# Kernel optimization log

Hardware: AMD Instinct MI355X
Metric: run time of the kernel (lower is better)

Reference implementation:

```python
import math
import jax, jax.numpy as jnp
import numpy as np

ALPHA = 0.2                         # LeakyReLU slope
LAMBDA_INIT = 0.8 - 0.6 * math.exp(-0.3 * 1)  # lambda_init_fn(depth=1)
NEG_INF = -9e15
EPS_LN = 1e-5

B, N, IN_F, OUT_F = 4, 2048, 512, 512
INTERNAL = OUT_F // 2
REL_DIM = 10
NUM_REL = 6


def setup_inputs() -> dict:
    key = jax.random.key(0)
    ks = jax.random.split(key, 16)
    xav = lambda k, shape, fan: jax.random.normal(k, shape, jnp.float32) * (1.414 * math.sqrt(2.0 / fan))
    h = jax.random.normal(ks[0], (B, N, IN_F), jnp.float32)
    adj = jax.random.randint(ks[1], (B, N, N), 0, NUM_REL, jnp.int32)
    W = xav(ks[2], (IN_F, OUT_F), IN_F + OUT_F)
    a_left_pos = xav(ks[3], (INTERNAL,), INTERNAL + 1)
    a_right_pos = xav(ks[4], (INTERNAL,), INTERNAL + 1)
    a_left_neg = xav(ks[5], (INTERNAL,), INTERNAL + 1)
    a_right_neg = xav(ks[6], (INTERNAL,), INTERNAL + 1)
    rel_table = jax.random.normal(ks[7], (NUM_REL, REL_DIM), jnp.float32)
    a_rel_pos = xav(ks[8], (REL_DIM,), REL_DIM + 1)
    a_rel_neg = xav(ks[9], (REL_DIM,), REL_DIM + 1)
    ll1 = 0.1 * jax.random.normal(ks[10], (INTERNAL,), jnp.float32)
    lr1 = 0.1 * jax.random.normal(ks[11], (INTERNAL,), jnp.float32)
    ll2 = 0.1 * jax.random.normal(ks[12], (INTERNAL,), jnp.float32)
    lr2 = 0.1 * jax.random.normal(ks[13], (INTERNAL,), jnp.float32)
    ln_gamma = jnp.ones((OUT_F,), jnp.float32)
    ln_beta = jnp.zeros((OUT_F,), jnp.float32)
    return dict(h=h, adj=adj, W=W, a_left_pos=a_left_pos, a_right_pos=a_right_pos,
                a_left_neg=a_left_neg, a_right_neg=a_right_neg, rel_table=rel_table,
                a_rel_pos=a_rel_pos, a_rel_neg=a_rel_neg, ll1=ll1, lr1=lr1,
                ll2=ll2, lr2=lr2, ln_gamma=ln_gamma, ln_beta=ln_beta)


def _leaky(x):
    return jnp.where(x >= 0, x, ALPHA * x)


def reference(h, adj, W, a_left_pos, a_right_pos, a_left_neg, a_right_neg,
              rel_table, a_rel_pos, a_rel_neg, ll1, lr1, ll2, lr2,
              ln_gamma, ln_beta):
    # Projection: Wh [B,N,out] -> split into pos/neg halves [B,N,internal]
    Wh = jnp.einsum('bni,io->bno', h, W)
    Bn, Nn, _ = Wh.shape
    Wh2 = Wh.reshape(Bn, Nn, 2, INTERNAL)
    Wh_pos, Wh_neg = Wh2[:, :, 0, :], Wh2[:, :, 1, :]

    # Additive GAT-style scores: e[b,i,j] = a_left.Wh[i] + a_right.Wh[j]
    e_pos = (Wh_pos @ a_left_pos)[:, :, None] + (Wh_pos @ a_right_pos)[:, None, :]
    e_neg = (Wh_neg @ a_left_neg)[:, :, None] + (Wh_neg @ a_right_neg)[:, None, :]

    # Relation-embedding bias: gather [B,N,N,rel_dim] then project to scalar
    rel_emb = rel_table[adj]                       # [B,N,N,R]
    e_pos = e_pos + rel_emb @ a_rel_pos
    e_neg = e_neg + rel_emb @ a_rel_neg

    mask = adj > 0
    att_pos = jax.nn.softmax(jnp.where(mask, _leaky(e_pos), NEG_INF), axis=2)
    att_neg = jax.nn.softmax(jnp.where(mask, _leaky(e_neg), NEG_INF), axis=2)

    lam = jnp.exp(jnp.sum(ll1 * lr1)) - jnp.exp(jnp.sum(ll2 * lr2)) + LAMBDA_INIT
    attention = att_pos - lam * att_neg            # dropout is identity (eval)

    Wh_v = jnp.concatenate([Wh_pos, Wh_neg], axis=-1)   # [B,N,out]
    h_prime = jnp.einsum('bij,bjd->bid', attention, Wh_v)

    mu = jnp.mean(h_prime, axis=-1, keepdims=True)
    var = jnp.mean(jnp.square(h_prime - mu), axis=-1, keepdims=True)
    h_prime = (h_prime - mu) / jnp.sqrt(var + EPS_LN) * ln_gamma + ln_beta
    h_prime = h_prime * (1 - LAMBDA_INIT)
    return jax.nn.gelu(h_prime, approximate=False), attention
```

## Files before the change

kernel.cpp:

```cpp
#include <hip/hip_runtime.h>
#include <hip/hip_bf16.h>


#define B_ 4
#define N_ 2048
#define F_ 512
#define ALPHA_ 0.2f
#define NEG_INF_ -9000000000000000.0f
#define EPS_LN_ 1e-5f

typedef __attribute__((ext_vector_type(8))) short bf16x8;
typedef __attribute__((ext_vector_type(4))) float f32x4;

#define HBF_OFF   0
#define WHT_OFF   0
#define WT_OFF    8388608
#define WH_OFF    8912896
#define HP_OFF    8912896
#define ATTBF_OFF 25690112
#define EL_OFF    59244544
#define SC_OFF    59375616
#define FLAG_OFF  59375680
#define CANON_OFF 59375744

#define C_ALP 0
#define C_ARP 256
#define C_ALN 512
#define C_ARN 768
#define C_REL 1024
#define C_ARELP 1084
#define C_ARELN 1094
#define C_LL1 1104
#define C_LR1 1360
#define C_LL2 1616
#define C_LR2 1872
#define C_GAM 2128
#define C_BET 2640

__device__ __forceinline__ float bf_as_f32(unsigned short u) {
    return __uint_as_float(((unsigned)u) << 16);
}
__device__ __forceinline__ float ldf(const void* p, long i, int isf32) {
    return isf32 ? ((const float*)p)[i] : bf_as_f32(((const unsigned short*)p)[i]);
}

__global__ void k_detect(const unsigned short* __restrict__ hraw, int* __restrict__ flag) {
    __shared__ float wmax[4];
    int tid = threadIdx.x, lane = tid & 63, wid = tid >> 6;
    float mx = 0.f;
    for (int i = tid; i < 8192; i += 256) {
        float v = fabsf(bf_as_f32(hraw[i]));
        if (v == v && v > mx) mx = v;
    }
    for (int off = 32; off; off >>= 1) mx = fmaxf(mx, __shfl_down(mx, off));
    if (lane == 0) wmax[wid] = mx;
    __syncthreads();
    if (tid == 0) {
        float m = fmaxf(fmaxf(wmax[0], wmax[1]), fmaxf(wmax[2], wmax[3]));
        flag[0] = (m > 1e10f) ? 1 : 0;
    }
}

__global__ __launch_bounds__(256) void k_conv_h(const void* __restrict__ h, const int* __restrict__ flag,
                                                __hip_bfloat16* __restrict__ hbf) {
    int fl = flag[0];
    int idx = blockIdx.x * 256 + threadIdx.x;
    hbf[idx] = __float2bfloat16(ldf(h, idx, fl));
}

__global__ __launch_bounds__(256) void k_conv_W(const void* __restrict__ W, const int* __restrict__ flag,
                                                __hip_bfloat16* __restrict__ Wt) {
    int fl = flag[0];
    int idx = blockIdx.x * 256 + threadIdx.x;
    int k = idx >> 9, o = idx & 511;
    Wt[o * 512 + k] = __float2bfloat16(ldf(W, idx, fl));
}

__global__ void k_conv_small(const void* alp, const void* arp, const void* aln, const void* arn,
                             const void* rel, const void* arelp, const void* areln,
                             const void* ll1, const void* lr1, const void* ll2, const void* lr2,
                             const void* gam, const void* bet,
                             const int* __restrict__ flag, float* __restrict__ canon) {
    int fl = flag[0];
    int tid = threadIdx.x;
    canon[C_ALP + tid] = ldf(alp, tid, fl);
    canon[C_ARP + tid] = ldf(arp, tid, fl);
    canon[C_ALN + tid] = ldf(aln, tid, fl);
    canon[C_ARN + tid] = ldf(arn, tid, fl);
    canon[C_LL1 + tid] = ldf(ll1, tid, fl);
    canon[C_LR1 + tid] = ldf(lr1, tid, fl);
    canon[C_LL2 + tid] = ldf(ll2, tid, fl);
    canon[C_LR2 + tid] = ldf(lr2, tid, fl);
    canon[C_GAM + tid] = ldf(gam, tid, fl);
    canon[C_GAM + 256 + tid] = ldf(gam, 256 + tid, fl);
    canon[C_BET + tid] = ldf(bet, tid, fl);
    canon[C_BET + 256 + tid] = ldf(bet, 256 + tid, fl);
    if (tid < 60) canon[C_REL + tid] = ldf(rel, tid, fl);
    if (tid < 10) { canon[C_ARELP + tid] = ldf(arelp, tid, fl); canon[C_ARELN + tid] = ldf(areln, tid, fl); }
}

__global__ void k_scalars(const float* __restrict__ canon, float* __restrict__ sc) {
    int lane = threadIdx.x;
    float s1 = 0.f, s2 = 0.f;
    for (int k = lane; k < 256; k += 64) {
        s1 += canon[C_LL1 + k] * canon[C_LR1 + k];
        s2 += canon[C_LL2 + k] * canon[C_LR2 + k];
    }
    for (int off = 32; off; off >>= 1) { s1 += __shfl_down(s1, off); s2 += __shfl_down(s2, off); }
    if (lane == 0) {
        float lam_init = 0.8f - 0.6f * expf(-0.3f);
        sc[0] = expf(s1) - expf(s2) + lam_init;
    }
    if (lane < 6) {
        float p = 0.f, n = 0.f;
        for (int d = 0; d < 10; ++d) {
            float rv = canon[C_REL + lane * 10 + d];
            p += rv * canon[C_ARELP + d];
            n += rv * canon[C_ARELN + d];
        }
        sc[1 + lane] = p;
        sc[7 + lane] = n;
    }
}

__global__ __launch_bounds__(256) void k_gemm_wh(const __hip_bfloat16* __restrict__ A,
                                                 const __hip_bfloat16* __restrict__ Bt,
                                                 float* __restrict__ C) {
    __shared__ short As[128][32];
    __shared__ short Bs[64][32];
    int tid = threadIdx.x, wid = tid >> 6, lane = tid & 63;
    int bm = blockIdx.x * 128, bn = blockIdx.y * 64;
    const short* Ag = (const short*)A;
    const short* Bg = (const short*)Bt;
    f32x4 acc[2][4] = {};
    for (int k0 = 0; k0 < 512; k0 += 32) {
        __syncthreads();
#pragma unroll
        for (int it = 0; it < 2; ++it) {
            int t = it * 256 + tid;
            int row = t >> 2, col8 = (t & 3) * 8;
            *(bf16x8*)&As[row][col8] = *(const bf16x8*)&Ag[(bm + row) * 512 + k0 + col8];
        }
        {
            int row = tid >> 2, col8 = (tid & 3) * 8;
            *(bf16x8*)&Bs[row][col8] = *(const bf16x8*)&Bg[(bn + row) * 512 + k0 + col8];
        }
        __syncthreads();
        int l15 = lane & 15, kh = (lane >> 4) * 8;
        bf16x8 af[2], bfr[4];
#pragma unroll
        for (int m = 0; m < 2; ++m) af[m] = *(const bf16x8*)&As[wid * 32 + m * 16 + l15][kh];
#pragma unroll
        for (int n = 0; n < 4; ++n) bfr[n] = *(const bf16x8*)&Bs[n * 16 + l15][kh];
#pragma unroll
        for (int m = 0; m < 2; ++m)
#pragma unroll
            for (int n = 0; n < 4; ++n)
                acc[m][n] = __builtin_amdgcn_mfma_f32_16x16x32_bf16(af[m], bfr[n], acc[m][n], 0, 0, 0);
    }
    int l15 = lane & 15, rg = (lane >> 4) * 4;
#pragma unroll
    for (int m = 0; m < 2; ++m)
#pragma unroll
        for (int n = 0; n < 4; ++n)
#pragma unroll
            for (int r = 0; r < 4; ++r) {
                int row = bm + wid * 32 + m * 16 + rg + r;
                int col = bn + n * 16 + l15;
                C[row * 512 + col] = acc[m][n][r];
            }
}

__global__ __launch_bounds__(256) void k_transWh(const float* __restrict__ Wh, __hip_bfloat16* __restrict__ Wht) {
    __shared__ float t[32][33];
    int b = blockIdx.z;
    int o0 = blockIdx.x * 32, j0 = blockIdx.y * 32;
    int tx = threadIdx.x & 31, ty = threadIdx.x >> 5;
#pragma unroll
    for (int r = 0; r < 4; ++r) {
        int j = j0 + ty + r * 8;
        t[ty + r * 8][tx] = Wh[(b * 2048 + j) * 512 + o0 + tx];
    }
    __syncthreads();
#pragma unroll
    for (int r = 0; r < 4; ++r) {
        int o = o0 + ty + r * 8;
        Wht[((long)b * 512 + o) * 2048 + j0 + tx] = __float2bfloat16(t[tx][ty + r * 8]);
    }
}

__global__ __launch_bounds__(256) void k_edots(const float* __restrict__ Wh, const float* __restrict__ canon,
                                               float* __restrict__ el) {
    int wid = threadIdx.x >> 6, lane = threadIdx.x & 63;
    int m = blockIdx.x * 4 + wid;
    float selp = 0.f, serp = 0.f, seln = 0.f, sern = 0.f;
#pragma unroll
    for (int t = 0; t < 4; ++t) {
        int k = t * 64 + lane;
        float wp = Wh[m * 512 + k];
        float wn = Wh[m * 512 + 256 + k];
        selp += wp * canon[C_ALP + k];
        serp += wp * canon[C_ARP + k];
        seln += wn * canon[C_ALN + k];
        sern += wn * canon[C_ARN + k];
    }
    for (int off = 32; off; off >>= 1) {
        selp += __shfl_down(selp, off); serp += __shfl_down(serp, off);
        seln += __shfl_down(seln, off); sern += __shfl_down(sern, off);
    }
    if (lane == 0) {
        el[m] = selp; el[8192 + m] = serp; el[16384 + m] = seln; el[24576 + m] = sern;
    }
}

__global__ __launch_bounds__(256) void k_attn(const int* __restrict__ adj,
                                              const float* __restrict__ el, const float* __restrict__ sc,
                                              float* __restrict__ att_f32,
                                              __hip_bfloat16* __restrict__ att_bf) {
    __shared__ float s_rp[6], s_rn[6], s_lam[1];
    __shared__ float rmp[4], rmn[4], rsp[4], rsn[4];
    int tid = threadIdx.x, lane = tid & 63, wid = tid >> 6;
    if (tid < 6) { s_rp[tid] = sc[1 + tid]; s_rn[tid] = sc[7 + tid]; }
    if (tid == 6) s_lam[0] = sc[0];
    int m = blockIdx.x, b = m >> 11;
    float elp = el[m], eln = el[16384 + m];
    const float* erp = el + 8192 + b * 2048;
    const float* ern = el + 24576 + b * 2048;
    const int* adjr = adj + (long)m * 2048;
    __syncthreads();
    float sp[8], sn[8];
    float mp = NEG_INF_, mn = NEG_INF_;
#pragma unroll
    for (int t = 0; t < 8; ++t) {
        int j = t * 256 + tid;
        int a = adjr[j];
        float ep = elp + erp[j] + s_rp[a];
        float en = eln + ern[j] + s_rn[a];
        ep = ep >= 0.f ? ep : ALPHA_ * ep;
        en = en >= 0.f ? en : ALPHA_ * en;
        sp[t] = a > 0 ? ep : NEG_INF_;
        sn[t] = a > 0 ? en : NEG_INF_;
        mp = fmaxf(mp, sp[t]); mn = fmaxf(mn, sn[t]);
    }
    for (int off = 32; off; off >>= 1) { mp = fmaxf(mp, __shfl_down(mp, off)); mn = fmaxf(mn, __shfl_down(mn, off)); }
    if (lane == 0) { rmp[wid] = mp; rmn[wid] = mn; }
    __syncthreads();
    mp = fmaxf(fmaxf(rmp[0], rmp[1]), fmaxf(rmp[2], rmp[3]));
    mn = fmaxf(fmaxf(rmn[0], rmn[1]), fmaxf(rmn[2], rmn[3]));
    float sump = 0.f, sumn = 0.f;
#pragma unroll
    for (int t = 0; t < 8; ++t) {
        sp[t] = expf(sp[t] - mp);
        sn[t] = expf(sn[t] - mn);
        sump += sp[t]; sumn += sn[t];
    }
    for (int off = 32; off; off >>= 1) { sump += __shfl_down(sump, off); sumn += __shfl_down(sumn, off); }
    if (lane == 0) { rsp[wid] = sump; rsn[wid] = sumn; }
    __syncthreads();
    sump = rsp[0] + rsp[1] + rsp[2] + rsp[3];
    sumn = rsn[0] + rsn[1] + rsn[2] + rsn[3];
    float ip = 1.0f / sump, inn = 1.0f / sumn;
    float lam = s_lam[0];
#pragma unroll
    for (int t = 0; t < 8; ++t) {
        float v = sp[t] * ip - lam * sn[t] * inn;
        long idx = (long)m * 2048 + t * 256 + tid;
        att_f32[idx] = v;
        att_bf[idx] = __float2bfloat16(v);
    }
}

__global__ __launch_bounds__(256) void k_hprime(const __hip_bfloat16* __restrict__ att,
                                                const __hip_bfloat16* __restrict__ Wht,
                                                float* __restrict__ HP) {
    __shared__ short As[128][32];
    __shared__ short Bs[64][32];
    int tid = threadIdx.x, wid = tid >> 6, lane = tid & 63;
    int b = blockIdx.z;
    int bm = blockIdx.x * 128, bn = blockIdx.y * 64;
    const short* Ag = (const short*)(att + (long)b * 2048 * 2048);
    const short* Bg = (const short*)(Wht + (long)b * 512 * 2048);
    f32x4 acc[2][4] = {};
    for (int k0 = 0; k0 < 2048; k0 += 32) {
        __syncthreads();
#pragma unroll
        for (int it = 0; it < 2; ++it) {
            int t = it * 256 + tid;
            int row = t >> 2, col8 = (t & 3) * 8;
            *(bf16x8*)&As[row][col8] = *(const bf16x8*)&Ag[(long)(bm + row) * 2048 + k0 + col8];
        }
        {
            int row = tid >> 2, col8 = (tid & 3) * 8;
            *(bf16x8*)&Bs[row][col8] = *(const bf16x8*)&Bg[(long)(bn + row) * 2048 + k0 + col8];
        }
        __syncthreads();
        int l15 = lane & 15, kh = (lane >> 4) * 8;
        bf16x8 af[2], bfr[4];
#pragma unroll
        for (int m = 0; m < 2; ++m) af[m] = *(const bf16x8*)&As[wid * 32 + m * 16 + l15][kh];
#pragma unroll
        for (int n = 0; n < 4; ++n) bfr[n] = *(const bf16x8*)&Bs[n * 16 + l15][kh];
#pragma unroll
        for (int m = 0; m < 2; ++m)
#pragma unroll
            for (int n = 0; n < 4; ++n)
                acc[m][n] = __builtin_amdgcn_mfma_f32_16x16x32_bf16(af[m], bfr[n], acc[m][n], 0, 0, 0);
    }
    int l15 = lane & 15, rg = (lane >> 4) * 4;
#pragma unroll
    for (int m = 0; m < 2; ++m)
#pragma unroll
        for (int n = 0; n < 4; ++n)
#pragma unroll
            for (int r = 0; r < 4; ++r) {
                int row = bm + wid * 32 + m * 16 + rg + r;
                int col = bn + n * 16 + l15;
                HP[((long)b * 2048 + row) * 512 + col] = acc[m][n][r];
            }
}

__global__ __launch_bounds__(256) void k_lngelu(const float* __restrict__ HP, const float* __restrict__ canon,
                                                float* __restrict__ out) {
    int wid = threadIdx.x >> 6, lane = threadIdx.x & 63;
    int m = blockIdx.x * 4 + wid;
    float x[8]; float s = 0.f, ss = 0.f;
#pragma unroll
    for (int t = 0; t < 8; ++t) {
        x[t] = HP[m * 512 + t * 64 + lane];
        s += x[t]; ss += x[t] * x[t];
    }
    for (int off = 32; off; off >>= 1) { s += __shfl_xor(s, off); ss += __shfl_xor(ss, off); }
    float mu = s * (1.0f / 512.0f);
    float var = ss * (1.0f / 512.0f) - mu * mu;
    float inv = rsqrtf(fmaxf(var, 0.0f) + EPS_LN_);
    float scale = 1.0f - (0.8f - 0.6f * expf(-0.3f));
#pragma unroll
    for (int t = 0; t < 8; ++t) {
        int k = t * 64 + lane;
        float y = (x[t] - mu) * inv * canon[C_GAM + k] + canon[C_BET + k];
        y *= scale;
        float g = 0.5f * y * (1.0f + erff(y * 0.70710678118654752f));
        out[m * 512 + k] = g;
    }
}

extern "C" void kernel_launch(void* const* d_in, const int* in_sizes, int n_in,
                              void* d_out, int out_size, void* d_ws, size_t ws_size,
                              hipStream_t stream) {
    const void* h   = d_in[0];
    const int*  adj = (const int*)d_in[1];
    const void* W   = d_in[2];
    const void* alp = d_in[3];
    const void* arp = d_in[4];
    const void* aln = d_in[5];
    const void* arn = d_in[6];
    const void* rel = d_in[7];
    const void* arelp = d_in[8];
    const void* areln = d_in[9];
    const void* ll1 = d_in[10];
    const void* lr1 = d_in[11];
    const void* ll2 = d_in[12];
    const void* lr2 = d_in[13];
    const void* gam = d_in[14];
    const void* bet = d_in[15];

    char* ws = (char*)d_ws;
    __hip_bfloat16* hbf   = (__hip_bfloat16*)(ws + HBF_OFF);
    __hip_bfloat16* Wt    = (__hip_bfloat16*)(ws + WT_OFF);
    float*          Wh    = (float*)(ws + WH_OFF);
    __hip_bfloat16* Wht   = (__hip_bfloat16*)(ws + WHT_OFF);
    __hip_bfloat16* attbf = (__hip_bfloat16*)(ws + ATTBF_OFF);
    float*          el    = (float*)(ws + EL_OFF);
    float*          sc    = (float*)(ws + SC_OFF);
    int*            flg   = (int*)(ws + FLAG_OFF);
    float*          can   = (float*)(ws + CANON_OFF);
    float*          HP    = (float*)(ws + HP_OFF);

    float* out_gelu = (float*)d_out;
    float* out_att  = out_gelu + (size_t)B_ * N_ * F_;

    k_detect<<<1, 256, 0, stream>>>((const unsigned short*)h, flg);
    k_conv_h<<<16384, 256, 0, stream>>>(h, flg, hbf);
    k_conv_W<<<1024, 256, 0, stream>>>(W, flg, Wt);
    k_conv_small<<<1, 256, 0, stream>>>(alp, arp, aln, arn, rel, arelp, areln,
                                        ll1, lr1, ll2, lr2, gam, bet, flg, can);
    k_scalars<<<1, 64, 0, stream>>>(can, sc);
    k_gemm_wh<<<dim3(64, 8), 256, 0, stream>>>(hbf, Wt, Wh);
    k_transWh<<<dim3(16, 64, 4), 256, 0, stream>>>(Wh, Wht);
    k_edots<<<2048, 256, 0, stream>>>(Wh, can, el);
    k_attn<<<8192, 256, 0, stream>>>(adj, el, sc, out_att, attbf);
    k_hprime<<<dim3(16, 8, 4), 256, 0, stream>>>(attbf, Wht, HP);
    k_lngelu<<<2048, 256, 0, stream>>>(HP, can, out_gelu);
}
```

Before: 286.0 us.

## Merge prep kernels, vectorize conversions, and use 128x128 GEMM tiles with direct-to-LDS loads

Folds the detect, small-parameter conversion and scalar kernels into one prep kernel. The h conversion is vectorized to 8 elements per thread, and the W transpose now goes through a shared-memory tile. Both GEMMs use a shared 128x128 tile kernel that loads global memory straight into LDS with global_load_lds, and softmax switches to fast __expf. Larger tiles raise reuse per block but halve the grid of the h' GEMM to 256 blocks, which may leave CUs underfilled, and there is still no double buffering.

```diff
diff --git a/kernel.cpp b/kernel.cpp
--- a/kernel.cpp
+++ b/kernel.cpp
@@ -27,13 +27,6 @@
 #define C_ARP 256
 #define C_ALN 512
 #define C_ARN 768
-#define C_REL 1024
-#define C_ARELP 1084
-#define C_ARELN 1094
-#define C_LL1 1104
-#define C_LR1 1360
-#define C_LL2 1616
-#define C_LR2 1872
 #define C_GAM 2128
 #define C_BET 2640
 
@@ -43,9 +36,23 @@
 __device__ __forceinline__ float ldf(const void* p, long i, int isf32) {
     return isf32 ? ((const float*)p)[i] : bf_as_f32(((const unsigned short*)p)[i]);
 }
-
-__global__ void k_detect(const unsigned short* __restrict__ hraw, int* __restrict__ flag) {
+__device__ __forceinline__ short f2bf(float f) {
+    __hip_bfloat16 t = __float2bfloat16(f);
+    return *reinterpret_cast<short*>(&t);
+}
+
+#define GLL16(g, l) __builtin_amdgcn_global_load_lds( \
+    (const __attribute__((address_space(1))) void*)(g), \
+    (__attribute__((address_space(3))) void*)(l), 16, 0, 0)
+
+__global__ void k_prep(const unsigned short* __restrict__ hraw,
+                       const void* alp, const void* arp, const void* aln, const void* arn,
+                       const void* rel, const void* arelp, const void* areln,
+                       const void* ll1, const void* lr1, const void* ll2, const void* lr2,
+                       const void* gam, const void* bet,
+                       int* __restrict__ flag, float* __restrict__ canon, float* __restrict__ sc) {
     __shared__ float wmax[4];
+    __shared__ int s_fl;
     int tid = threadIdx.x, lane = tid & 63, wid = tid >> 6;
     float mx = 0.f;
     for (int i = tid; i < 8192; i += 256) {
@@ -57,117 +64,117 @@
     __syncthreads();
     if (tid == 0) {
         float m = fmaxf(fmaxf(wmax[0], wmax[1]), fmaxf(wmax[2], wmax[3]));
-        flag[0] = (m > 1e10f) ? 1 : 0;
-    }
-}
-
-__global__ __launch_bounds__(256) void k_conv_h(const void* __restrict__ h, const int* __restrict__ flag,
-                                                __hip_bfloat16* __restrict__ hbf) {
-    int fl = flag[0];
-    int idx = blockIdx.x * 256 + threadIdx.x;
-    hbf[idx] = __float2bfloat16(ldf(h, idx, fl));
-}
-
-__global__ __launch_bounds__(256) void k_conv_W(const void* __restrict__ W, const int* __restrict__ flag,
-                                                __hip_bfloat16* __restrict__ Wt) {
-    int fl = flag[0];
-    int idx = blockIdx.x * 256 + threadIdx.x;
-    int k = idx >> 9, o = idx & 511;
-    Wt[o * 512 + k] = __float2bfloat16(ldf(W, idx, fl));
-}
-
-__global__ void k_conv_small(const void* alp, const void* arp, const void* aln, const void* arn,
-                             const void* rel, const void* arelp, const void* areln,
-                             const void* ll1, const void* lr1, const void* ll2, const void* lr2,
-                             const void* gam, const void* bet,
-                             const int* __restrict__ flag, float* __restrict__ canon) {
-    int fl = flag[0];
-    int tid = threadIdx.x;
+        int f = (m > 1e10f) ? 1 : 0;
+        s_fl = f; flag[0] = f;
+    }
+    __syncthreads();
+    int fl = s_fl;
     canon[C_ALP + tid] = ldf(alp, tid, fl);
     canon[C_ARP + tid] = ldf(arp, tid, fl);
     canon[C_ALN + tid] = ldf(aln, tid, fl);
     canon[C_ARN + tid] = ldf(arn, tid, fl);
-    canon[C_LL1 + tid] = ldf(ll1, tid, fl);
-    canon[C_LR1 + tid] = ldf(lr1, tid, fl);
-    canon[C_LL2 + tid] = ldf(ll2, tid, fl);
-    canon[C_LR2 + tid] = ldf(lr2, tid, fl);
     canon[C_GAM + tid] = ldf(gam, tid, fl);
     canon[C_GAM + 256 + tid] = ldf(gam, 256 + tid, fl);
     canon[C_BET + tid] = ldf(bet, tid, fl);
     canon[C_BET + 256 + tid] = ldf(bet, 256 + tid, fl);
-    if (tid < 60) canon[C_REL + tid] = ldf(rel, tid, fl);
-    if (tid < 10) { canon[C_ARELP + tid] = ldf(arelp, tid, fl); canon[C_ARELN + tid] = ldf(areln, tid, fl); }
-}
-
-__global__ void k_scalars(const float* __restrict__ canon, float* __restrict__ sc) {
-    int lane = threadIdx.x;
-    float s1 = 0.f, s2 = 0.f;
-    for (int k = lane; k < 256; k += 64) {
-        s1 += canon[C_LL1 + k] * canon[C_LR1 + k];
-        s2 += canon[C_LL2 + k] * canon[C_LR2 + k];
-    }
-    for (int off = 32; off; off >>= 1) { s1 += __shfl_down(s1, off); s2 += __shfl_down(s2, off); }
-    if (lane == 0) {
-        float lam_init = 0.8f - 0.6f * expf(-0.3f);
-        sc[0] = expf(s1) - expf(s2) + lam_init;
-    }
-    if (lane < 6) {
+    if (wid == 0) {
+        float s1 = 0.f, s2 = 0.f;
+        for (int k = lane; k < 256; k += 64) {
+            s1 += ldf(ll1, k, fl) * ldf(lr1, k, fl);
+            s2 += ldf(ll2, k, fl) * ldf(lr2, k, fl);
+        }
+        for (int off = 32; off; off >>= 1) { s1 += __shfl_down(s1, off); s2 += __shfl_down(s2, off); }
+        if (lane == 0) {
+            float lam_init = 0.8f - 0.6f * expf(-0.3f);
+            sc[0] = expf(s1) - expf(s2) + lam_init;
+        }
+    } else if (wid == 1 && lane < 6) {
         float p = 0.f, n = 0.f;
         for (int d = 0; d < 10; ++d) {
-            float rv = canon[C_REL + lane * 10 + d];
-            p += rv * canon[C_ARELP + d];
-            n += rv * canon[C_ARELN + d];
+            float rv = ldf(rel, lane * 10 + d, fl);
+            p += rv * ldf(arelp, d, fl);
+            n += rv * ldf(areln, d, fl);
         }
         sc[1 + lane] = p;
         sc[7 + lane] = n;
     }
 }
 
-__global__ __launch_bounds__(256) void k_gemm_wh(const __hip_bfloat16* __restrict__ A,
-                                                 const __hip_bfloat16* __restrict__ Bt,
-                                                 float* __restrict__ C) {
-    __shared__ short As[128][32];
-    __shared__ short Bs[64][32];
+__global__ __launch_bounds__(256) void k_conv_h8(const void* __restrict__ h, const int* __restrict__ flag,
+                                                 short* __restrict__ hbf) {
+    int fl = flag[0];
+    int i = (blockIdx.x * 256 + threadIdx.x) * 8;
+    bf16x8 v;
+    if (fl) {
+        const float4* p = (const float4*)((const float*)h + i);
+        float4 a = p[0], b = p[1];
+        v[0] = f2bf(a.x); v[1] = f2bf(a.y); v[2] = f2bf(a.z); v[3] = f2bf(a.w);
+        v[4] = f2bf(b.x); v[5] = f2bf(b.y); v[6] = f2bf(b.z); v[7] = f2bf(b.w);
+    } else {
+        v = *(const bf16x8*)((const short*)h + i);
+    }
+    *(bf16x8*)(hbf + i) = v;
+}
+
+__global__ __launch_bounds__(256) void k_transW(const void* __restrict__ W, const int* __restrict__ flag,
+                                                __hip_bfloat16* __restrict__ Wt) {
+    __shared__ float t[32][33];
+    int fl = flag[0];
+    int k0 = blockIdx.x * 32, o0 = blockIdx.y * 32;
+    int tx = threadIdx.x & 31, ty = threadIdx.x >> 5;
+#pragma unroll
+    for (int r = 0; r < 4; ++r)
+        t[ty + r * 8][tx] = ldf(W, (k0 + ty + r * 8) * 512 + o0 + tx, fl);
+    __syncthreads();
+#pragma unroll
+    for (int r = 0; r < 4; ++r)
+        Wt[(o0 + ty + r * 8) * 512 + k0 + tx] = __float2bfloat16(t[tx][ty + r * 8]);
+}
+
+__global__ __launch_bounds__(256) void k_gemm128(const short* __restrict__ A, const short* __restrict__ B,
+                                                 float* __restrict__ C, int K, int N,
+                                                 long aBatch, long bBatch, long cBatch) {
+    __shared__ short As[128 * 32];
+    __shared__ short Bs[128 * 32];
     int tid = threadIdx.x, wid = tid >> 6, lane = tid & 63;
-    int bm = blockIdx.x * 128, bn = blockIdx.y * 64;
-    const short* Ag = (const short*)A;
-    const short* Bg = (const short*)Bt;
-    f32x4 acc[2][4] = {};
-    for (int k0 = 0; k0 < 512; k0 += 32) {
+    int bm = blockIdx.x * 128, bn = blockIdx.y * 128;
+    int bz = blockIdx.z;
+    const short* Ab = A + bz * aBatch + (long)bm * K;
+    const short* Bb = B + bz * bBatch + (long)bn * K;
+    f32x4 acc[4][4] = {};
+    int wr = (wid >> 1) * 64, wc = (wid & 1) * 64;
+    int c0 = wid * 64 + lane, c1 = c0 + 256;
+    int r0 = c0 >> 2, q0 = (c0 & 3) * 8;
+    int r1 = c1 >> 2, q1 = (c1 & 3) * 8;
+    int l15 = lane & 15, kh = (lane >> 4) * 8;
+    for (int k0 = 0; k0 < K; k0 += 32) {
         __syncthreads();
-#pragma unroll
-        for (int it = 0; it < 2; ++it) {
-            int t = it * 256 + tid;
-            int row = t >> 2, col8 = (t & 3) * 8;
-            *(bf16x8*)&As[row][col8] = *(const bf16x8*)&Ag[(bm + row) * 512 + k0 + col8];
-        }
-        {
-            int row = tid >> 2, col8 = (tid & 3) * 8;
-            *(bf16x8*)&Bs[row][col8] = *(const bf16x8*)&Bg[(bn + row) * 512 + k0 + col8];
-        }
+        GLL16(Ab + (long)r0 * K + k0 + q0, As + c0 * 8);
+        GLL16(Ab + (long)r1 * K + k0 + q1, As + c1 * 8);
+        GLL16(Bb + (long)r0 * K + k0 + q0, Bs + c0 * 8);
+        GLL16(Bb + (long)r1 * K + k0 + q1, Bs + c1 * 8);
         __syncthreads();
-        int l15 = lane & 15, kh = (lane >> 4) * 8;
-        bf16x8 af[2], bfr[4];
-#pragma unroll
-        for (int m = 0; m < 2; ++m) af[m] = *(const bf16x8*)&As[wid * 32 + m * 16 + l15][kh];
-#pragma unroll
-        for (int n = 0; n < 4; ++n) bfr[n] = *(const bf16x8*)&Bs[n * 16 + l15][kh];
-#pragma unroll
-        for (int m = 0; m < 2; ++m)
+        bf16x8 af[4], bq[4];
+#pragma unroll
+        for (int m = 0; m < 4; ++m) af[m] = *(const bf16x8*)&As[(wr + m * 16 + l15) * 32 + kh];
+#pragma unroll
+        for (int n = 0; n < 4; ++n) bq[n] = *(const bf16x8*)&Bs[(wc + n * 16 + l15) * 32 + kh];
+#pragma unroll
+        for (int m = 0; m < 4; ++m)
 #pragma unroll
             for (int n = 0; n < 4; ++n)
-                acc[m][n] = __builtin_amdgcn_mfma_f32_16x16x32_bf16(af[m], bfr[n], acc[m][n], 0, 0, 0);
-    }
-    int l15 = lane & 15, rg = (lane >> 4) * 4;
-#pragma unroll
-    for (int m = 0; m < 2; ++m)
+                acc[m][n] = __builtin_amdgcn_mfma_f32_16x16x32_bf16(af[m], bq[n], acc[m][n], 0, 0, 0);
+    }
+    int rg = (lane >> 4) * 4;
+#pragma unroll
+    for (int m = 0; m < 4; ++m)
 #pragma unroll
         for (int n = 0; n < 4; ++n)
 #pragma unroll
             for (int r = 0; r < 4; ++r) {
-                int row = bm + wid * 32 + m * 16 + rg + r;
-                int col = bn + n * 16 + l15;
-                C[row * 512 + col] = acc[m][n][r];
+                int row = bm + wr + m * 16 + rg + r;
+                int col = bn + wc + n * 16 + l15;
+                C[bz * cBatch + (long)row * N + col] = acc[m][n][r];
             }
 }
 
@@ -177,16 +184,12 @@
     int o0 = blockIdx.x * 32, j0 = blockIdx.y * 32;
     int tx = threadIdx.x & 31, ty = threadIdx.x >> 5;
 #pragma unroll
-    for (int r = 0; r < 4; ++r) {
-        int j = j0 + ty + r * 8;
-        t[ty + r * 8][tx] = Wh[(b * 2048 + j) * 512 + o0 + tx];
-    }
-    __syncthreads();
-#pragma unroll
-    for (int r = 0; r < 4; ++r) {
-        int o = o0 + ty + r * 8;
-        Wht[((long)b * 512 + o) * 2048 + j0 + tx] = __float2bfloat16(t[tx][ty + r * 8]);
-    }
+    for (int r = 0; r < 4; ++r)
+        t[ty + r * 8][tx] = Wh[(b * 2048 + j0 + ty + r * 8) * 512 + o0 + tx];
+    __syncthreads();
+#pragma unroll
+    for (int r = 0; r < 4; ++r)
+        Wht[((long)b * 512 + o0 + ty + r * 8) * 2048 + j0 + tx] = __float2bfloat16(t[tx][ty + r * 8]);
 }
 
 __global__ __launch_bounds__(256) void k_edots(const float* __restrict__ Wh, const float* __restrict__ canon,
@@ -250,8 +253,8 @@
     float sump = 0.f, sumn = 0.f;
 #pragma unroll
     for (int t = 0; t < 8; ++t) {
-        sp[t] = expf(sp[t] - mp);
-        sn[t] = expf(sn[t] - mn);
+        sp[t] = __expf(sp[t] - mp);
+        sn[t] = __expf(sn[t] - mn);
         sump += sp[t]; sumn += sn[t];
     }
     for (int off = 32; off; off >>= 1) { sump += __shfl_down(sump, off); sumn += __shfl_down(sumn, off); }
@@ -268,55 +271,6 @@
         att_f32[idx] = v;
         att_bf[idx] = __float2bfloat16(v);
     }
-}
-
-__global__ __launch_bounds__(256) void k_hprime(const __hip_bfloat16* __restrict__ att,
-                                                const __hip_bfloat16* __restrict__ Wht,
-                                                float* __restrict__ HP) {
-    __shared__ short As[128][32];
-    __shared__ short Bs[64][32];
-    int tid = threadIdx.x, wid = tid >> 6, lane = tid & 63;
-    int b = blockIdx.z;
-    int bm = blockIdx.x * 128, bn = blockIdx.y * 64;
-    const short* Ag = (const short*)(att + (long)b * 2048 * 2048);
-    const short* Bg = (const short*)(Wht + (long)b * 512 * 2048);
-    f32x4 acc[2][4] = {};
-    for (int k0 = 0; k0 < 2048; k0 += 32) {
-        __syncthreads();
-#pragma unroll
-        for (int it = 0; it < 2; ++it) {
-            int t = it * 256 + tid;
-            int row = t >> 2, col8 = (t & 3) * 8;
-            *(bf16x8*)&As[row][col8] = *(const bf16x8*)&Ag[(long)(bm + row) * 2048 + k0 + col8];
-        }
-        {
-            int row = tid >> 2, col8 = (tid & 3) * 8;
-            *(bf16x8*)&Bs[row][col8] = *(const bf16x8*)&Bg[(long)(bn + row) * 2048 + k0 + col8];
-        }
-        __syncthreads();
-        int l15 = lane & 15, kh = (lane >> 4) * 8;
-        bf16x8 af[2], bfr[4];
-#pragma unroll
-        for (int m = 0; m < 2; ++m) af[m] = *(const bf16x8*)&As[wid * 32 + m * 16 + l15][kh];
-#pragma unroll
-        for (int n = 0; n < 4; ++n) bfr[n] = *(const bf16x8*)&Bs[n * 16 + l15][kh];
-#pragma unroll
-        for (int m = 0; m < 2; ++m)
-#pragma unroll
-            for (int n = 0; n < 4; ++n)
-                acc[m][n] = __builtin_amdgcn_mfma_f32_16x16x32_bf16(af[m], bfr[n], acc[m][n], 0, 0, 0);
-    }
-    int l15 = lane & 15, rg = (lane >> 4) * 4;
-#pragma unroll
-    for (int m = 0; m < 2; ++m)
-#pragma unroll
-        for (int n = 0; n < 4; ++n)
-#pragma unroll
-            for (int r = 0; r < 4; ++r) {
-                int row = bm + wid * 32 + m * 16 + rg + r;
-                int col = bn + n * 16 + l15;
-                HP[((long)b * 2048 + row) * 512 + col] = acc[m][n][r];
-            }
 }
 
 __global__ __launch_bounds__(256) void k_lngelu(const float* __restrict__ HP, const float* __restrict__ canon,
@@ -350,22 +304,9 @@
     const void* h   = d_in[0];
     const int*  adj = (const int*)d_in[1];
     const void* W   = d_in[2];
-    const void* alp = d_in[3];
-    const void* arp = d_in[4];
-    const void* aln = d_in[5];
-    const void* arn = d_in[6];
-    const void* rel = d_in[7];
-    const void* arelp = d_in[8];
-    const void* areln = d_in[9];
-    const void* ll1 = d_in[10];
-    const void* lr1 = d_in[11];
-    const void* ll2 = d_in[12];
-    const void* lr2 = d_in[13];
-    const void* gam = d_in[14];
-    const void* bet = d_in[15];
 
     char* ws = (char*)d_ws;
-    __hip_bfloat16* hbf   = (__hip_bfloat16*)(ws + HBF_OFF);
+    short*          hbf   = (short*)(ws + HBF_OFF);
     __hip_bfloat16* Wt    = (__hip_bfloat16*)(ws + WT_OFF);
     float*          Wh    = (float*)(ws + WH_OFF);
     __hip_bfloat16* Wht   = (__hip_bfloat16*)(ws + WHT_OFF);
@@ -379,16 +320,17 @@
     float* out_gelu = (float*)d_out;
     float* out_att  = out_gelu + (size_t)B_ * N_ * F_;
 
-    k_detect<<<1, 256, 0, stream>>>((const unsigned short*)h, flg);
-    k_conv_h<<<16384, 256, 0, stream>>>(h, flg, hbf);
-    k_conv_W<<<1024, 256, 0, stream>>>(W, flg, Wt);
-    k_conv_small<<<1, 256, 0, stream>>>(alp, arp, aln, arn, rel, arelp, areln,
-                                        ll1, lr1, ll2, lr2, gam, bet, flg, can);
-    k_scalars<<<1, 64, 0, stream>>>(can, sc);
-    k_gemm_wh<<<dim3(64, 8), 256, 0, stream>>>(hbf, Wt, Wh);
+    k_prep<<<1, 256, 0, stream>>>((const unsigned short*)h,
+                                  d_in[3], d_in[4], d_in[5], d_in[6], d_in[7], d_in[8], d_in[9],
+                                  d_in[10], d_in[11], d_in[12], d_in[13], d_in[14], d_in[15],
+                                  flg, can, sc);
+    k_conv_h8<<<2048, 256, 0, stream>>>(h, flg, hbf);
+    k_transW<<<dim3(16, 16), 256, 0, stream>>>(W, flg, Wt);
+    k_gemm128<<<dim3(64, 4, 1), 256, 0, stream>>>(hbf, (const short*)Wt, Wh, 512, 512, 0, 0, 0);
     k_transWh<<<dim3(16, 64, 4), 256, 0, stream>>>(Wh, Wht);
     k_edots<<<2048, 256, 0, stream>>>(Wh, can, el);
     k_attn<<<8192, 256, 0, stream>>>(adj, el, sc, out_att, attbf);
-    k_hprime<<<dim3(16, 8, 4), 256, 0, stream>>>(attbf, Wht, HP);
+    k_gemm128<<<dim3(16, 4, 4), 256, 0, stream>>>((const short*)attbf, (const short*)Wht, HP, 2048, 512,
+                                                  2048L * 2048, 512L * 2048, 2048L * 512);
     k_lngelu<<<2048, 256, 0, stream>>>(HP, can, out_gelu);
 }
```

Result: no change. 287.7 us (+0.6%).
